# Kernel tuning notes

Hardware: AMD Instinct MI355X
Metric: run time of the kernel (lower is better)

Reference implementation:

```python
import jax, jax.numpy as jnp
import numpy as np

B, S, D = 4, 1024, 1280
H, DH = 20, 64          # n_head, d_hidden = embed_dim // n_head
DF = 4 * D              # r_ff = 4


def setup_inputs() -> dict:
    key = jax.random.key(0)
    ks = jax.random.split(key, 8)
    s_qkv = 1.0 / np.sqrt(D)
    inp = {
        "x": jax.random.normal(ks[0], (B, S, D), dtype=jnp.float32),
        # projection weights stored [in, out] so y = x @ W
        "Wq": jax.random.normal(ks[1], (D, H * DH), dtype=jnp.float32) * s_qkv,
        "Wk": jax.random.normal(ks[2], (D, H * DH), dtype=jnp.float32) * s_qkv,
        "Wv": jax.random.normal(ks[3], (D, H * DH), dtype=jnp.float32) * s_qkv,
        "ln_g": jnp.ones((D,), dtype=jnp.float32),
        "ln_b": jnp.zeros((D,), dtype=jnp.float32),
        "W1": jax.random.normal(ks[4], (D, DF), dtype=jnp.float32) * np.sqrt(2.0 / D),
        "b1": jnp.zeros((DF,), dtype=jnp.float32),
        "W2": jax.random.normal(ks[5], (DF, D), dtype=jnp.float32) * (1.0 / np.sqrt(DF)),
        "b2": jnp.zeros((D,), dtype=jnp.float32),
    }
    return inp


def reference(x, Wq, Wk, Wv, ln_g, ln_b, W1, b1, W2, b2):
    scaling = 1.0 / np.sqrt(DH)
    # --- Attention (note: original forward never applies to_out) ---
    q = (x @ Wq).reshape(B, S, H, DH) * scaling
    k = (x @ Wk).reshape(B, S, H, DH)
    v = (x @ Wv).reshape(B, S, H, DH)
    attn = jnp.einsum('bqhd,bkhd->bhqk', q, k)
    attn = jax.nn.softmax(attn, axis=-1)
    out = jnp.einsum('bhqk,bkhd->bqhd', attn, v).reshape(B, S, H * DH)
    x = out + x  # residual
    # --- FeedForward: LayerNorm -> linear1 -> relu -> linear2, residual ---
    mu = jnp.mean(x, axis=-1, keepdims=True)
    var = jnp.mean(jnp.square(x - mu), axis=-1, keepdims=True)
    h = (x - mu) * jax.lax.rsqrt(var + 1e-5) * ln_g + ln_b
    h = jax.nn.relu(h @ W1 + b1)
    h = h @ W2 + b2
    return x + h
```

## Files before the change

### kernel.cpp

```cpp
#include <hip/hip_runtime.h>
#include <hip/hip_bf16.h>

typedef short bf16x8 __attribute__((ext_vector_type(8)));
typedef float f32x4 __attribute__((ext_vector_type(4)));

typedef unsigned int u32_as1 __attribute__((address_space(1)));
typedef unsigned int u32_as3 __attribute__((address_space(3)));

#define B_ 4
#define S_ 1024
#define D_ 1280
#define H_ 20
#define DH_ 64
#define DF_ 5120
#define BS_ (B_*S_)
#define NQKV 3840

__device__ __forceinline__ void gld_lds16(const __hip_bfloat16* g, __hip_bfloat16* l) {
  __builtin_amdgcn_global_load_lds((const u32_as1*)g, (u32_as3*)l, 16, 0, 0);
}

__global__ __launch_bounds__(256) void cvt_f2b(
    const float* __restrict__ in, __hip_bfloat16* __restrict__ out, int n4)
{
  int i = blockIdx.x * 256 + threadIdx.x;
  if (i >= n4) return;
  const float4 v = ((const float4*)in)[i];
  __hip_bfloat16 o[4] = {__float2bfloat16(v.x), __float2bfloat16(v.y),
                         __float2bfloat16(v.z), __float2bfloat16(v.w)};
  *(short4*)(out + (size_t)i * 4) = *(short4*)o;
}

__global__ __launch_bounds__(256) void transpose_f2b(
    const float* __restrict__ in, __hip_bfloat16* __restrict__ out,
    int K, int N)
{
  __shared__ float tile[32][33];
  int k0 = blockIdx.x * 32, n0 = blockIdx.y * 32;
  int tx = threadIdx.x & 31, ty = threadIdx.x >> 5;
  #pragma unroll
  for (int i = 0; i < 32; i += 8)
    tile[ty + i][tx] = in[(size_t)(k0 + ty + i) * N + n0 + tx];
  __syncthreads();
  #pragma unroll
  for (int i = 0; i < 32; i += 8)
    out[(size_t)(n0 + ty + i) * K + k0 + tx] = __float2bfloat16(tile[tx][ty + i]);
}

__global__ __launch_bounds__(256) void transpose_v(
    const __hip_bfloat16* __restrict__ qkv, __hip_bfloat16* __restrict__ vT)
{
  __shared__ __hip_bfloat16 tile[32][33];
  int s0 = blockIdx.x * 32;
  int d0 = blockIdx.y * 32;
  int bh = blockIdx.z;
  int b = bh / H_, h = bh - b * H_;
  int tx = threadIdx.x & 31, ty = threadIdx.x >> 5;
  const __hip_bfloat16* src = qkv + (size_t)b * S_ * NQKV + 2 * D_ + h * DH_;
  #pragma unroll
  for (int i = 0; i < 32; i += 8)
    tile[ty + i][tx] = src[(size_t)(s0 + ty + i) * NQKV + d0 + tx];
  __syncthreads();
  __hip_bfloat16* dst = vT + (size_t)bh * DH_ * S_;
  #pragma unroll
  for (int i = 0; i < 32; i += 8)
    dst[(size_t)(d0 + ty + i) * S_ + s0 + tx] = tile[tx][ty + i];
}

template<int EPI>
__global__ __launch_bounds__(512, 2) void gemm256(
    const __hip_bfloat16* __restrict__ A,
    const __hip_bfloat16* __restrict__ BT,
    const float* __restrict__ bias,
    __hip_bfloat16* __restrict__ C,
    float* __restrict__ Cf0,
    float* __restrict__ Cf1,
    float* __restrict__ Cf2,
    int M, int N, int K, int KextA, int KextR)
{
  __shared__ __align__(16) __hip_bfloat16 As[2][2][256 * 32];
  __shared__ __align__(16) __hip_bfloat16 Bs[2][2][256 * 32];
  __hip_bfloat16* AsF = &As[0][0][0];
  __hip_bfloat16* BsF = &Bs[0][0][0];

  const int t = threadIdx.x;
  const int lane = t & 63;
  const int wave = t >> 6;
  const int wm = wave >> 2, wn = wave & 3;
  const int quad = lane >> 4, l16 = lane & 15;

  const int gx = gridDim.x;
  const int nwg = gx * gridDim.y;
  int orig = blockIdx.y * gx + blockIdx.x;
  int bx = blockIdx.x, by = blockIdx.y;
  if ((nwg & 7) == 0) {
    const int q = nwg >> 3;
    const int swz = (orig & 7) * q + (orig >> 3);
    bx = swz % gx; by = swz / gx;
  }
  const int bm = bx * 256, bn = by * 256;

  const int z = blockIdx.z;
  const int koff = (z == 0) ? 0 : (KextA + (z - 1) * KextR);
  const int Kc = (z == 0) ? KextA : KextR;
  const int NT = Kc >> 6;

  const int srow = t >> 2;
  const int sc = (t & 3) ^ ((t >> 3) & 3);
  const __hip_bfloat16* Ag = A  + (size_t)(bm + srow) * K + koff + sc * 8;
  const __hip_bfloat16* Bg = BT + (size_t)(bn + srow) * K + koff + sc * 8;
  const size_t rq = (size_t)128 * K;

  const int swzf = quad ^ ((l16 >> 1) & 3);
  const int aob = (wm * 128 + l16) * 32 + swzf * 8;
  const int bob = (wn * 64 + l16) * 32 + swzf * 8;

  f32x4 acc[8][4];
  #pragma unroll
  for (int i = 0; i < 8; i++)
    #pragma unroll
    for (int j = 0; j < 4; j++)
      acc[i][j] = (f32x4){0.f, 0.f, 0.f, 0.f};

#define STAGE_A(u_, kk_, b_) do { \
    const __hip_bfloat16* g_ = Ag + (size_t)(u_) * 64 + (kk_) * 32; \
    gld_lds16(g_,      AsF + ((b_) * 2 + (kk_)) * 8192 + t * 8); \
    gld_lds16(g_ + rq, AsF + ((b_) * 2 + (kk_)) * 8192 + 4096 + t * 8); \
  } while (0)
#define STAGE_B(u_, kk_, b_) do { \
    const __hip_bfloat16* g_ = Bg + (size_t)(u_) * 64 + (kk_) * 32; \
    gld_lds16(g_,      BsF + ((b_) * 2 + (kk_)) * 8192 + t * 8); \
    gld_lds16(g_ + rq, BsF + ((b_) * 2 + (kk_)) * 8192 + 4096 + t * 8); \
  } while (0)

  STAGE_A(0, 0, 0); STAGE_B(0, 0, 0); STAGE_A(0, 1, 0); STAGE_B(0, 1, 0);
  STAGE_B(1, 0, 1); STAGE_A(1, 0, 1); STAGE_B(1, 1, 1);
  asm volatile("s_waitcnt vmcnt(6)" ::: "memory");
  __builtin_amdgcn_s_barrier();
  asm volatile("" ::: "memory");

  bf16x8 av[4], bv[4];

#define PHASE_MFMA(ibase_) \
    __builtin_amdgcn_s_barrier(); \
    asm volatile("s_waitcnt lgkmcnt(0)" ::: "memory"); \
    __builtin_amdgcn_s_setprio(1); \
    _Pragma("unroll") \
    for (int i = 0; i < 4; i++) \
      _Pragma("unroll") \
      for (int j = 0; j < 4; j++) \
        acc[(ibase_) + i][j] = __builtin_amdgcn_mfma_f32_16x16x32_bf16(av[i], bv[j], acc[(ibase_) + i][j], 0, 0, 0); \
    __builtin_amdgcn_s_setprio(0); \
    __builtin_amdgcn_s_barrier(); \
    asm volatile("" ::: "memory");

#define TILE_BODY(u_, B_) do { \
    const int hb0 = (B_) * 2 * 8192, hb1 = ((B_) * 2 + 1) * 8192; \
     \
    _Pragma("unroll") \
    for (int i = 0; i < 4; i++) av[i] = *(const bf16x8*)(AsF + hb0 + aob + i * 512); \
    _Pragma("unroll") \
    for (int j = 0; j < 4; j++) bv[j] = *(const bf16x8*)(BsF + hb0 + bob + j * 512); \
    if ((u_) + 1 < NT) STAGE_A((u_) + 1, 1, (B_) ^ 1); \
    PHASE_MFMA(0) \
     \
    _Pragma("unroll") \
    for (int i = 0; i < 4; i++) av[i] = *(const bf16x8*)(AsF + hb0 + aob + (i + 4) * 512); \
    if ((u_) + 2 < NT) STAGE_B((u_) + 2, 0, (B_)); \
    PHASE_MFMA(4) \
     \
    _Pragma("unroll") \
    for (int i = 0; i < 4; i++) av[i] = *(const bf16x8*)(AsF + hb1 + aob + i * 512); \
    _Pragma("unroll") \
    for (int j = 0; j < 4; j++) bv[j] = *(const bf16x8*)(BsF + hb1 + bob + j * 512); \
    if ((u_) + 2 < NT) STAGE_A((u_) + 2, 0, (B_)); \
    PHASE_MFMA(0) \
     \
    _Pragma("unroll") \
    for (int i = 0; i < 4; i++) av[i] = *(const bf16x8*)(AsF + hb1 + aob + (i + 4) * 512); \
    if ((u_) + 2 < NT) { \
      STAGE_B((u_) + 2, 1, (B_)); \
      asm volatile("s_waitcnt vmcnt(6)" ::: "memory"); \
    } else { \
      asm volatile("s_waitcnt vmcnt(0)" ::: "memory"); \
    } \
    PHASE_MFMA(4) \
  } while (0)

  for (int u = 0; u < NT; u += 2) {
    TILE_BODY(u, 0);
    TILE_BODY(u + 1, 1);
  }

#undef TILE_BODY
#undef PHASE_MFMA
#undef STAGE_A
#undef STAGE_B

  float* Cf = (z == 0) ? Cf0 : ((z == 1) ? Cf1 : Cf2);
  #pragma unroll
  for (int i = 0; i < 8; i++) {
    #pragma unroll
    for (int j = 0; j < 4; j++) {
      int col = bn + wn * 64 + j * 16 + l16;
      #pragma unroll
      for (int r = 0; r < 4; r++) {
        int row = bm + wm * 128 + i * 16 + quad * 4 + r;
        float v = acc[i][j][r];
        if (EPI == 1) { v += bias[col]; v = fmaxf(v, 0.f); }
        if (EPI == 3) {
          Cf[(size_t)row * N + col] = v;
        } else {
          C[(size_t)row * N + col] = __float2bfloat16(v);
        }
      }
    }
  }
}

__global__ __launch_bounds__(256) void ffn2_reduce3(
    const float* __restrict__ P0, const float* __restrict__ P1,
    const float* __restrict__ bias, const float* __restrict__ resid,
    float* __restrict__ out)
{
  int i = blockIdx.x * 256 + threadIdx.x;
  float4 p0 = ((const float4*)P0)[i];
  float4 p1 = ((const float4*)P1)[i];
  float4 p2 = ((const float4*)out)[i];
  float4 r  = ((const float4*)resid)[i];
  float4 b  = ((const float4*)bias)[i % (D_ / 4)];
  float4 o;
  o.x = p0.x + p1.x + p2.x + r.x + b.x;
  o.y = p0.y + p1.y + p2.y + r.y + b.y;
  o.z = p0.z + p1.z + p2.z + r.z + b.z;
  o.w = p0.w + p1.w + p2.w + r.w + b.w;
  ((float4*)out)[i] = o;
}

__global__ __launch_bounds__(256) void attn_mfma(
    const __hip_bfloat16* __restrict__ qkv,
    const __hip_bfloat16* __restrict__ vT,
    const float* __restrict__ x,
    float* __restrict__ x1)
{
  const int qt = blockIdx.x, h = blockIdx.y, b = blockIdx.z;
  const int t = threadIdx.x;
  const int lane = t & 63;
  const int wave = t >> 6;
  const int quad = lane >> 4, l16 = lane & 15;

  __shared__ __hip_bfloat16 Ks[2][64 * 64];
  __shared__ __hip_bfloat16 Vs[2][64 * 64];
  __shared__ short Pl[4][16][72];

  const int qrow0 = qt * 128 + wave * 32;
  const size_t tok0 = (size_t)b * S_;
  const int qcol = h * DH_;
  const int kcol = D_ + h * DH_;
  const size_t vtbase = (size_t)(b * H_ + h) * DH_ * S_;

  const int s1i = t + 256;
  const int r0 = t >> 3,   c0 = (t & 7)   ^ (r0 & 7);
  const int r1 = s1i >> 3, c1 = (s1i & 7) ^ (r1 & 7);
  const __hip_bfloat16* Kg0 = qkv + (tok0 + r0) * NQKV + kcol + c0 * 8;
  const __hip_bfloat16* Kg1 = qkv + (tok0 + r1) * NQKV + kcol + c1 * 8;
  const __hip_bfloat16* Vg0 = vT + vtbase + (size_t)r0 * S_ + c0 * 8;
  const __hip_bfloat16* Vg1 = vT + vtbase + (size_t)r1 * S_ + c1 * 8;
  const size_t kstep = (size_t)64 * NQKV;

  const float qscale = 0.125f * 1.44269504088896340736f;
  bf16x8 aq[2][2];
  #pragma unroll
  for (int m = 0; m < 2; m++)
    #pragma unroll
    for (int kc = 0; kc < 2; kc++) {
      bf16x8 raw = *(const bf16x8*)(qkv + (tok0 + qrow0 + m * 16 + l16) * NQKV
                                        + qcol + kc * 32 + quad * 8);
      bf16x8 scaled;
      #pragma unroll
      for (int j = 0; j < 8; j++) {
        float f = __uint_as_float(((unsigned)(unsigned short)raw[j]) << 16) * qscale;
        __hip_bfloat16 hb = __float2bfloat16(f);
        scaled[j] = *reinterpret_cast<short*>(&hb);
      }
      aq[m][kc] = scaled;
    }

  f32x4 O[2][4];
  float lsum[2][4];
  #pragma unroll
  for (int m = 0; m < 2; m++)
    #pragma unroll
    for (int n = 0; n < 4; n++) O[m][n] = (f32x4){0.f, 0.f, 0.f, 0.f};
  #pragma unroll
  for (int m = 0; m < 2; m++)
    #pragma unroll
    for (int r = 0; r < 4; r++) lsum[m][r] = 0.f;

  gld_lds16(Kg0, &Ks[0][t * 8]);
  gld_lds16(Kg1, &Ks[0][t * 8 + 2048]);
  gld_lds16(Vg0, &Vs[0][t * 8]);
  gld_lds16(Vg1, &Vs[0][t * 8 + 2048]);

  const int fsw = l16 & 7;

  for (int kt = 0; kt < S_ / 64; kt++) {
    const int buf = kt & 1;
    __syncthreads();

    if (kt + 1 < S_ / 64) {
      const int nb = buf ^ 1;
      gld_lds16(Kg0 + (size_t)(kt + 1) * kstep, &Ks[nb][t * 8]);
      gld_lds16(Kg1 + (size_t)(kt + 1) * kstep, &Ks[nb][t * 8 + 2048]);
      gld_lds16(Vg0 + (kt + 1) * 64, &Vs[nb][t * 8]);
      gld_lds16(Vg1 + (kt + 1) * 64, &Vs[nb][t * 8 + 2048]);
    }

    bf16x8 kb[4][2];
    #pragma unroll
    for (int j = 0; j < 4; j++)
      #pragma unroll
      for (int kc = 0; kc < 2; kc++)
        kb[j][kc] = *(const bf16x8*)&Ks[buf][(j * 16 + l16) * 64
                                            + (((kc * 4 + quad) ^ fsw) * 8)];
    f32x4 sc[2][4];
    #pragma unroll
    for (int m = 0; m < 2; m++)
      #pragma unroll
      for (int j = 0; j < 4; j++) {
        sc[m][j] = (f32x4){0.f, 0.f, 0.f, 0.f};
        sc[m][j] = __builtin_amdgcn_mfma_f32_16x16x32_bf16(aq[m][0], kb[j][0], sc[m][j], 0, 0, 0);
        sc[m][j] = __builtin_amdgcn_mfma_f32_16x16x32_bf16(aq[m][1], kb[j][1], sc[m][j], 0, 0, 0);
      }

    bf16x8 vb[4][2];
    #pragma unroll
    for (int n = 0; n < 4; n++)
      #pragma unroll
      for (int kc = 0; kc < 2; kc++)
        vb[n][kc] = *(const bf16x8*)&Vs[buf][(n * 16 + l16) * 64
                                            + (((kc * 4 + quad) ^ fsw) * 8)];

    #pragma unroll
    for (int m = 0; m < 2; m++) {
      #pragma unroll
      for (int j = 0; j < 4; j++)
        #pragma unroll
        for (int r = 0; r < 4; r++) {
          float p = exp2f(sc[m][j][r]);
          lsum[m][r] += p;
          Pl[wave][quad * 4 + r][j * 16 + l16] = (short)(__float_as_uint(p) >> 16);
        }
      bf16x8 pa0 = *(const bf16x8*)&Pl[wave][l16][quad * 8];
      bf16x8 pa1 = *(const bf16x8*)&Pl[wave][l16][32 + quad * 8];
      #pragma unroll
      for (int n = 0; n < 4; n++) {
        O[m][n] = __builtin_amdgcn_mfma_f32_16x16x32_bf16(pa0, vb[n][0], O[m][n], 0, 0, 0);
        O[m][n] = __builtin_amdgcn_mfma_f32_16x16x32_bf16(pa1, vb[n][1], O[m][n], 0, 0, 0);
      }
    }
  }

  #pragma unroll
  for (int m = 0; m < 2; m++)
    #pragma unroll
    for (int r = 0; r < 4; r++) {
      float s = lsum[m][r];
      s += __shfl_xor(s, 1);
      s += __shfl_xor(s, 2);
      s += __shfl_xor(s, 4);
      s += __shfl_xor(s, 8);
      lsum[m][r] = 1.f / s;
    }

  #pragma unroll
  for (int m = 0; m < 2; m++)
    #pragma unroll
    for (int n = 0; n < 4; n++)
      #pragma unroll
      for (int r = 0; r < 4; r++) {
        size_t row = tok0 + qrow0 + m * 16 + quad * 4 + r;
        int col = qcol + n * 16 + l16;
        size_t idx = row * D_ + col;
        x1[idx] = O[m][n][r] * lsum[m][r] + x[idx];
      }
}

__global__ __launch_bounds__(256) void ln_kernel(
    const float* __restrict__ x1, const float* __restrict__ g,
    const float* __restrict__ bta, __hip_bfloat16* __restrict__ h)
{
  int row = blockIdx.x, t = threadIdx.x;
  __shared__ float red[256];
  float v[5];
  size_t base = (size_t)row * D_;
  #pragma unroll
  for (int i = 0; i < 5; i++) v[i] = x1[base + t + 256 * i];
  float s = v[0] + v[1] + v[2] + v[3] + v[4];
  red[t] = s; __syncthreads();
  for (int off = 128; off; off >>= 1) {
    if (t < off) red[t] += red[t + off];
    __syncthreads();
  }
  float mu = red[0] * (1.f / D_);
  __syncthreads();
  float sq = 0.f;
  #pragma unroll
  for (int i = 0; i < 5; i++) { float d = v[i] - mu; sq += d * d; }
  red[t] = sq; __syncthreads();
  for (int off = 128; off; off >>= 1) {
    if (t < off) red[t] += red[t + off];
    __syncthreads();
  }
  float rs = rsqrtf(red[0] * (1.f / D_) + 1e-5f);
  #pragma unroll
  for (int i = 0; i < 5; i++) {
    int c = t + 256 * i;
    float hv = (v[i] - mu) * rs * g[c] + bta[c];
    h[base + c] = __float2bfloat16(hv);
  }
}

extern "C" void kernel_launch(void* const* d_in, const int* in_sizes, int n_in,
                              void* d_out, int out_size, void* d_ws, size_t ws_size,
                              hipStream_t stream) {
  (void)in_sizes; (void)n_in; (void)out_size; (void)ws_size;
  const float* x   = (const float*)d_in[0];
  const float* Wq  = (const float*)d_in[1];
  const float* Wk  = (const float*)d_in[2];
  const float* Wv  = (const float*)d_in[3];
  const float* lng = (const float*)d_in[4];
  const float* lnb = (const float*)d_in[5];
  const float* W1  = (const float*)d_in[6];
  const float* b1  = (const float*)d_in[7];
  const float* W2  = (const float*)d_in[8];
  const float* b2  = (const float*)d_in[9];
  float* out = (float*)d_out;

  char* ws = (char*)d_ws;
  size_t o = 0;
  __hip_bfloat16* W2T = (__hip_bfloat16*)(ws + o); o += (size_t)D_ * DF_ * 2;
  float*          x1  = (float*)(ws + o);          o += (size_t)BS_ * D_ * 4;
  char* regA = ws + o; o += (size_t)DF_ * D_ * 2 + (size_t)BS_ * D_ * 2;
  __hip_bfloat16* W1T  = (__hip_bfloat16*)regA;
  __hip_bfloat16* hbuf = (__hip_bfloat16*)(regA + (size_t)DF_ * D_ * 2);
  float*          P0   = (float*)regA;
  char* regB = ws + o;
  __hip_bfloat16* xb    = (__hip_bfloat16*)regB;
  __hip_bfloat16* BTqkv = (__hip_bfloat16*)(regB + (size_t)BS_ * D_ * 2);
  __hip_bfloat16* qkv   = (__hip_bfloat16*)(regB + (size_t)BS_ * D_ * 2
                                                 + (size_t)NQKV * D_ * 2);
  __hip_bfloat16* vT    = (__hip_bfloat16*)(regB + (size_t)BS_ * D_ * 2
                                                 + (size_t)NQKV * D_ * 2
                                                 + (size_t)BS_ * NQKV * 2);
  float*          P1    = (float*)regB;
  __hip_bfloat16* gbuf  = (__hip_bfloat16*)(regB + (size_t)BS_ * D_ * 4);
  float*          P2    = out;

  transpose_f2b<<<dim3(D_/32, D_/32), 256, 0, stream>>>(Wq, BTqkv,                   D_, D_);
  transpose_f2b<<<dim3(D_/32, D_/32), 256, 0, stream>>>(Wk, BTqkv + (size_t)D_*D_,   D_, D_);
  transpose_f2b<<<dim3(D_/32, D_/32), 256, 0, stream>>>(Wv, BTqkv + (size_t)2*D_*D_, D_, D_);
  transpose_f2b<<<dim3(D_/32, DF_/32), 256, 0, stream>>>(W1, W1T, D_, DF_);
  transpose_f2b<<<dim3(DF_/32, D_/32), 256, 0, stream>>>(W2, W2T, DF_, D_);
  cvt_f2b<<<(BS_*D_/4 + 255)/256, 256, 0, stream>>>(x, xb, BS_*D_/4);

  gemm256<0><<<dim3(BS_/256, NQKV/256), 512, 0, stream>>>(
      xb, BTqkv, nullptr, qkv, nullptr, nullptr, nullptr, BS_, NQKV, D_, D_, D_);
  transpose_v<<<dim3(S_/32, DH_/32, B_*H_), 256, 0, stream>>>(qkv, vT);
  attn_mfma<<<dim3(S_/128, H_, B_), 256, 0, stream>>>(qkv, vT, x, x1);
  ln_kernel<<<BS_, 256, 0, stream>>>(x1, lng, lnb, hbuf);
  gemm256<1><<<dim3(BS_/256, DF_/256), 512, 0, stream>>>(
      hbuf, W1T, b1, gbuf, nullptr, nullptr, nullptr, BS_, DF_, D_, D_, D_);
  gemm256<3><<<dim3(BS_/256, D_/256, 3), 512, 0, stream>>>(
      gbuf, W2T, nullptr, nullptr, P0, P1, P2, BS_, D_, DF_, 1792, 1664);
  ffn2_reduce3<<<BS_*D_/4/256, 256, 0, stream>>>(P0, P1, b2, x1, out);
}
```

Before: 410.4 us.

## Restructure GEMM to 4 waves with 128x128 per-wave tiles and simpler pipeline

The 256x256 GEMM drops from 8 waves (512 threads, 128x64 per wave) to 4 waves (256 threads, 128x128 per wave) with 8x8 accumulator fragments. It also replaces the fine-grained interleaved staging and per-phase barriers with a plain double-buffered loop: load fragments, issue the next tile's global-to-LDS copies, run 128 MFMAs, wait, then one barrier. The intent is fewer barriers and more MFMA work per LDS fragment read. The costs are a 256-register accumulator per thread, which limits occupancy to one block and may spill, and weaker latency hiding from the full vmcnt(0) wait each iteration.

```diff
diff --git a/kernel.cpp b/kernel.cpp
--- a/kernel.cpp
+++ b/kernel.cpp
@@ -68,7 +68,7 @@
 }
 
 template<int EPI>
-__global__ __launch_bounds__(512, 2) void gemm256(
+__global__ __launch_bounds__(256, 1) void gemm256(
     const __hip_bfloat16* __restrict__ A,
     const __hip_bfloat16* __restrict__ BT,
     const float* __restrict__ bias,
@@ -86,7 +86,7 @@
   const int t = threadIdx.x;
   const int lane = t & 63;
   const int wave = t >> 6;
-  const int wm = wave >> 2, wn = wave & 3;
+  const int wm = wave >> 1, wn = wave & 1;
   const int quad = lane >> 4, l16 = lane & 15;
 
   const int gx = gridDim.x;
@@ -105,104 +105,78 @@
   const int Kc = (z == 0) ? KextA : KextR;
   const int NT = Kc >> 6;
 
-  const int srow = t >> 2;
   const int sc = (t & 3) ^ ((t >> 3) & 3);
-  const __hip_bfloat16* Ag = A  + (size_t)(bm + srow) * K + koff + sc * 8;
-  const __hip_bfloat16* Bg = BT + (size_t)(bn + srow) * K + koff + sc * 8;
-  const size_t rq = (size_t)128 * K;
+  const __hip_bfloat16* Ag = A  + (size_t)(bm + (t >> 2)) * K + koff + sc * 8;
+  const __hip_bfloat16* Bg = BT + (size_t)(bn + (t >> 2)) * K + koff + sc * 8;
+  const size_t rq = (size_t)64 * K;
 
   const int swzf = quad ^ ((l16 >> 1) & 3);
   const int aob = (wm * 128 + l16) * 32 + swzf * 8;
-  const int bob = (wn * 64 + l16) * 32 + swzf * 8;
-
-  f32x4 acc[8][4];
+  const int bob = (wn * 128 + l16) * 32 + swzf * 8;
+
+  f32x4 acc[8][8];
   #pragma unroll
   for (int i = 0; i < 8; i++)
     #pragma unroll
-    for (int j = 0; j < 4; j++)
+    for (int j = 0; j < 8; j++)
       acc[i][j] = (f32x4){0.f, 0.f, 0.f, 0.f};
 
-#define STAGE_A(u_, kk_, b_) do { \
-    const __hip_bfloat16* g_ = Ag + (size_t)(u_) * 64 + (kk_) * 32; \
-    gld_lds16(g_,      AsF + ((b_) * 2 + (kk_)) * 8192 + t * 8); \
-    gld_lds16(g_ + rq, AsF + ((b_) * 2 + (kk_)) * 8192 + 4096 + t * 8); \
+#define STAGE(u_, bb_) do { \
+    const size_t co_ = (size_t)(u_) * 64; \
+    _Pragma("unroll") \
+    for (int q = 0; q < 4; q++) { \
+      gld_lds16(Ag + co_ + q * rq,      AsF + ((bb_) * 2 + 0) * 8192 + q * 2048 + t * 8); \
+      gld_lds16(Ag + co_ + 32 + q * rq, AsF + ((bb_) * 2 + 1) * 8192 + q * 2048 + t * 8); \
+      gld_lds16(Bg + co_ + q * rq,      BsF + ((bb_) * 2 + 0) * 8192 + q * 2048 + t * 8); \
+      gld_lds16(Bg + co_ + 32 + q * rq, BsF + ((bb_) * 2 + 1) * 8192 + q * 2048 + t * 8); \
+    } \
   } while (0)
-#define STAGE_B(u_, kk_, b_) do { \
-    const __hip_bfloat16* g_ = Bg + (size_t)(u_) * 64 + (kk_) * 32; \
-    gld_lds16(g_,      BsF + ((b_) * 2 + (kk_)) * 8192 + t * 8); \
-    gld_lds16(g_ + rq, BsF + ((b_) * 2 + (kk_)) * 8192 + 4096 + t * 8); \
-  } while (0)
-
-  STAGE_A(0, 0, 0); STAGE_B(0, 0, 0); STAGE_A(0, 1, 0); STAGE_B(0, 1, 0);
-  STAGE_B(1, 0, 1); STAGE_A(1, 0, 1); STAGE_B(1, 1, 1);
-  asm volatile("s_waitcnt vmcnt(6)" ::: "memory");
+
+  STAGE(0, 0);
+  asm volatile("s_waitcnt vmcnt(0)" ::: "memory");
   __builtin_amdgcn_s_barrier();
   asm volatile("" ::: "memory");
 
-  bf16x8 av[4], bv[4];
-
-#define PHASE_MFMA(ibase_) \
-    __builtin_amdgcn_s_barrier(); \
-    asm volatile("s_waitcnt lgkmcnt(0)" ::: "memory"); \
-    __builtin_amdgcn_s_setprio(1); \
-    _Pragma("unroll") \
-    for (int i = 0; i < 4; i++) \
-      _Pragma("unroll") \
-      for (int j = 0; j < 4; j++) \
-        acc[(ibase_) + i][j] = __builtin_amdgcn_mfma_f32_16x16x32_bf16(av[i], bv[j], acc[(ibase_) + i][j], 0, 0, 0); \
-    __builtin_amdgcn_s_setprio(0); \
-    __builtin_amdgcn_s_barrier(); \
+  for (int u = 0; u < NT; ++u) {
+    const int bb = u & 1;
+    const int hb0 = (bb * 2 + 0) * 8192, hb1 = (bb * 2 + 1) * 8192;
+
+    bf16x8 av[8], bv[8], aw[8], bw[8];
+    #pragma unroll
+    for (int mi = 0; mi < 8; mi++) av[mi] = *(const bf16x8*)(AsF + hb0 + aob + mi * 512);
+    #pragma unroll
+    for (int nj = 0; nj < 8; nj++) bv[nj] = *(const bf16x8*)(BsF + hb0 + bob + nj * 512);
+    if (u + 1 < NT) STAGE(u + 1, bb ^ 1);
+    #pragma unroll
+    for (int mi = 0; mi < 8; mi++) aw[mi] = *(const bf16x8*)(AsF + hb1 + aob + mi * 512);
+    #pragma unroll
+    for (int nj = 0; nj < 8; nj++) bw[nj] = *(const bf16x8*)(BsF + hb1 + bob + nj * 512);
+
+    #pragma unroll
+    for (int mi = 0; mi < 8; mi++)
+      #pragma unroll
+      for (int nj = 0; nj < 8; nj++)
+        acc[mi][nj] = __builtin_amdgcn_mfma_f32_16x16x32_bf16(av[mi], bv[nj], acc[mi][nj], 0, 0, 0);
+    #pragma unroll
+    for (int mi = 0; mi < 8; mi++)
+      #pragma unroll
+      for (int nj = 0; nj < 8; nj++)
+        acc[mi][nj] = __builtin_amdgcn_mfma_f32_16x16x32_bf16(aw[mi], bw[nj], acc[mi][nj], 0, 0, 0);
+
+    if (u + 1 < NT) { asm volatile("s_waitcnt vmcnt(0)" ::: "memory"); }
     asm volatile("" ::: "memory");
-
-#define TILE_BODY(u_, B_) do { \
-    const int hb0 = (B_) * 2 * 8192, hb1 = ((B_) * 2 + 1) * 8192; \
-     \
-    _Pragma("unroll") \
-    for (int i = 0; i < 4; i++) av[i] = *(const bf16x8*)(AsF + hb0 + aob + i * 512); \
-    _Pragma("unroll") \
-    for (int j = 0; j < 4; j++) bv[j] = *(const bf16x8*)(BsF + hb0 + bob + j * 512); \
-    if ((u_) + 1 < NT) STAGE_A((u_) + 1, 1, (B_) ^ 1); \
-    PHASE_MFMA(0) \
-     \
-    _Pragma("unroll") \
-    for (int i = 0; i < 4; i++) av[i] = *(const bf16x8*)(AsF + hb0 + aob + (i + 4) * 512); \
-    if ((u_) + 2 < NT) STAGE_B((u_) + 2, 0, (B_)); \
-    PHASE_MFMA(4) \
-     \
-    _Pragma("unroll") \
-    for (int i = 0; i < 4; i++) av[i] = *(const bf16x8*)(AsF + hb1 + aob + i * 512); \
-    _Pragma("unroll") \
-    for (int j = 0; j < 4; j++) bv[j] = *(const bf16x8*)(BsF + hb1 + bob + j * 512); \
-    if ((u_) + 2 < NT) STAGE_A((u_) + 2, 0, (B_)); \
-    PHASE_MFMA(0) \
-     \
-    _Pragma("unroll") \
-    for (int i = 0; i < 4; i++) av[i] = *(const bf16x8*)(AsF + hb1 + aob + (i + 4) * 512); \
-    if ((u_) + 2 < NT) { \
-      STAGE_B((u_) + 2, 1, (B_)); \
-      asm volatile("s_waitcnt vmcnt(6)" ::: "memory"); \
-    } else { \
-      asm volatile("s_waitcnt vmcnt(0)" ::: "memory"); \
-    } \
-    PHASE_MFMA(4) \
-  } while (0)
-
-  for (int u = 0; u < NT; u += 2) {
-    TILE_BODY(u, 0);
-    TILE_BODY(u + 1, 1);
-  }
-
-#undef TILE_BODY
-#undef PHASE_MFMA
-#undef STAGE_A
-#undef STAGE_B
+    __builtin_amdgcn_s_barrier();
+    asm volatile("" ::: "memory");
+  }
+
+#undef STAGE
 
   float* Cf = (z == 0) ? Cf0 : ((z == 1) ? Cf1 : Cf2);
   #pragma unroll
   for (int i = 0; i < 8; i++) {
     #pragma unroll
-    for (int j = 0; j < 4; j++) {
-      int col = bn + wn * 64 + j * 16 + l16;
+    for (int j = 0; j < 8; j++) {
+      int col = bn + wn * 128 + j * 16 + l16;
       #pragma unroll
       for (int r = 0; r < 4; r++) {
         int row = bm + wm * 128 + i * 16 + quad * 4 + r;
@@ -464,14 +438,14 @@
   transpose_f2b<<<dim3(DF_/32, D_/32), 256, 0, stream>>>(W2, W2T, DF_, D_);
   cvt_f2b<<<(BS_*D_/4 + 255)/256, 256, 0, stream>>>(x, xb, BS_*D_/4);
 
-  gemm256<0><<<dim3(BS_/256, NQKV/256), 512, 0, stream>>>(
+  gemm256<0><<<dim3(BS_/256, NQKV/256), 256, 0, stream>>>(
       xb, BTqkv, nullptr, qkv, nullptr, nullptr, nullptr, BS_, NQKV, D_, D_, D_);
   transpose_v<<<dim3(S_/32, DH_/32, B_*H_), 256, 0, stream>>>(qkv, vT);
   attn_mfma<<<dim3(S_/128, H_, B_), 256, 0, stream>>>(qkv, vT, x, x1);
   ln_kernel<<<BS_, 256, 0, stream>>>(x1, lng, lnb, hbuf);
-  gemm256<1><<<dim3(BS_/256, DF_/256), 512, 0, stream>>>(
+  gemm256<1><<<dim3(BS_/256, DF_/256), 256, 0, stream>>>(
       hbuf, W1T, b1, gbuf, nullptr, nullptr, nullptr, BS_, DF_, D_, D_, D_);
-  gemm256<3><<<dim3(BS_/256, D_/256, 3), 512, 0, stream>>>(
+  gemm256<3><<<dim3(BS_/256, D_/256, 3), 256, 0, stream>>>(
       gbuf, W2T, nullptr, nullptr, P0, P1, P2, BS_, D_, DF_, 1792, 1664);
   ffn2_reduce3<<<BS_*D_/4/256, 256, 0, stream>>>(P0, P1, b2, x1, out);
 }
```

Measured after the change: 443.3 us. +8.0%, slower.
